# Kernel optimization log

Measured on AMD Instinct MI355X. Metric: run time of the kernel, lower is better.

## Reference

```python
import jax, jax.numpy as jnp
import numpy as np

N_NODES = 100000
N_EDGES = 1600000
IN_DIM, HID_DIM, LAT_DIM = 256, 128, 64


def setup_inputs() -> dict:
    key = jax.random.key(0)
    ks = jax.random.split(key, 10)
    x = jax.random.normal(ks[0], (N_NODES, IN_DIM), dtype=jnp.float32)
    edge_index = jax.random.randint(ks[1], (2, N_EDGES), 0, N_NODES, dtype=jnp.int32)
    s = 1.0 / np.sqrt(IN_DIM)
    W1 = jax.random.normal(ks[2], (IN_DIM, HID_DIM), dtype=jnp.float32) * s
    b1 = jnp.zeros((HID_DIM,), dtype=jnp.float32)
    s2 = 1.0 / np.sqrt(HID_DIM)
    Wmu = jax.random.normal(ks[3], (HID_DIM, LAT_DIM), dtype=jnp.float32) * s2
    bmu = jnp.zeros((LAT_DIM,), dtype=jnp.float32)
    Wls = jax.random.normal(ks[4], (HID_DIM, LAT_DIM), dtype=jnp.float32) * s2
    bls = jnp.zeros((LAT_DIM,), dtype=jnp.float32)
    eps = jax.random.normal(ks[5], (N_NODES, LAT_DIM), dtype=jnp.float32)
    return {"x": x, "edge_index": edge_index, "W1": W1, "b1": b1,
            "Wmu": Wmu, "bmu": bmu, "Wls": Wls, "bls": bls, "eps": eps}


def _gcn_norm(edge_index, n_nodes):
    # PyG GCNConv: add self-loops, symmetric normalization D^-1/2 A D^-1/2
    loops = jnp.arange(n_nodes, dtype=edge_index.dtype)
    src = jnp.concatenate([edge_index[0], loops])
    dst = jnp.concatenate([edge_index[1], loops])
    ones = jnp.ones(src.shape[0], dtype=jnp.float32)
    deg = jax.ops.segment_sum(ones, dst, num_segments=n_nodes)
    dinv = jnp.where(deg > 0, jax.lax.rsqrt(deg), 0.0)
    norm = dinv[src] * dinv[dst]  # [E + N]
    return src, dst, norm


def _gcn_conv(x, src, dst, norm, W, b, n_nodes):
    h = x @ W                       # transform first (in_dim >= out_dim)
    msg = h[src] * norm[:, None]    # gather + scale per edge
    out = jax.ops.segment_sum(msg, dst, num_segments=n_nodes)  # scatter-add
    return out + b


def reference(x, edge_index, W1, b1, Wmu, bmu, Wls, bls, eps):
    n = x.shape[0]
    src, dst, norm = _gcn_norm(edge_index, n)
    hidden = jax.nn.relu(_gcn_conv(x, src, dst, norm, W1, b1, n))
    mu = _gcn_conv(hidden, src, dst, norm, Wmu, bmu, n)
    logstd = _gcn_conv(hidden, src, dst, norm, Wls, bls, n)
    # reparameterize (training mode): z = mu + eps * exp(logstd)
    z = mu + eps * jnp.exp(logstd)
    return (z, mu, logstd)
```

## Files before the change

### kernel.cpp

```cpp
#include <hip/hip_runtime.h>
#include <cstdint>
#include <cstddef>

typedef __attribute__((ext_vector_type(8))) short short8v;
typedef __attribute__((ext_vector_type(4))) float f32x4;

#define BSHIFT 9
#define NBUCK_MAX 256
#define BCAP 16384
#define F8SCALE 16.0f
#define F8INV   0.0625f

__device__ __forceinline__ unsigned short f2bf_rne(float x) {
    unsigned int u = __float_as_uint(x);
    return (unsigned short)((u + 0x7fffu + ((u >> 16) & 1u)) >> 16);
}
__device__ __forceinline__ float bflo(unsigned int u) { return __uint_as_float(u << 16); }
__device__ __forceinline__ float bfhi(unsigned int u) { return __uint_as_float(u & 0xffff0000u); }

__device__ __forceinline__ short8v pack_bf16x8(float4 a, float4 b) {
    unsigned int u0, u1, u2, u3;
    asm("v_cvt_pk_bf16_f32 %0, %1, %2" : "=v"(u0) : "v"(a.x), "v"(a.y));
    asm("v_cvt_pk_bf16_f32 %0, %1, %2" : "=v"(u1) : "v"(a.z), "v"(a.w));
    asm("v_cvt_pk_bf16_f32 %0, %1, %2" : "=v"(u2) : "v"(b.x), "v"(b.y));
    asm("v_cvt_pk_bf16_f32 %0, %1, %2" : "=v"(u3) : "v"(b.z), "v"(b.w));
    uint4 r = make_uint4(u0, u1, u2, u3);
    return *(short8v*)&r;
}

__device__ __forceinline__ unsigned int pk_fp8(float a, float b, float c, float d) {
    int r = 0;
    r = __builtin_amdgcn_cvt_pk_fp8_f32(a, b, r, false);
    r = __builtin_amdgcn_cvt_pk_fp8_f32(c, d, r, true);
    return (unsigned int)r;
}
__device__ __forceinline__ void accf8(float* a, uint2 v) {
    auto p0 = __builtin_amdgcn_cvt_pk_f32_fp8((int)v.x, false);
    auto p1 = __builtin_amdgcn_cvt_pk_f32_fp8((int)v.x, true);
    auto p2 = __builtin_amdgcn_cvt_pk_f32_fp8((int)v.y, false);
    auto p3 = __builtin_amdgcn_cvt_pk_f32_fp8((int)v.y, true);
    a[0] += p0[0]; a[1] += p0[1];
    a[2] += p1[0]; a[3] += p1[1];
    a[4] += p2[0]; a[5] += p2[1];
    a[6] += p3[0]; a[7] += p3[1];
}


__global__ __launch_bounds__(256) void k_scatb(const int* __restrict__ srcv,
                                               const int* __restrict__ dstv,
                                               int* __restrict__ bcur,
                                               unsigned int* __restrict__ ebuf, int E) {
    __shared__ int hcnt[NBUCK_MAX], hbase[NBUCK_MAX], hcur[NBUCK_MAX];
    int t = threadIdx.x;
    for (int b = t; b < NBUCK_MAX; b += 256) { hcnt[b] = 0; hcur[b] = 0; }
    __syncthreads();
    int base = blockIdx.x * 4096;
    for (int q = 0; q < 16; ++q) {
        int i = base + q * 256 + t;
        if (i < E) atomicAdd(&hcnt[dstv[i] >> BSHIFT], 1);
    }
    __syncthreads();
    for (int b = t; b < NBUCK_MAX; b += 256)
        hbase[b] = hcnt[b] ? atomicAdd(&bcur[b], hcnt[b]) : 0;
    __syncthreads();
    for (int q = 0; q < 16; ++q) {
        int i = base + q * 256 + t;
        if (i < E) {
            int d = dstv[i], b = d >> BSHIFT;
            int off = hbase[b] + atomicAdd(&hcur[b], 1);
            if (off < BCAP)
                ebuf[(size_t)b * BCAP + off] = ((unsigned)srcv[i] << 9) | (unsigned)(d & 511);
        }
    }
}

__global__ __launch_bounds__(512) void k_bsort(const unsigned int* __restrict__ ebuf,
                                               const int* __restrict__ bcur,
                                               int* __restrict__ colv,
                                               int* __restrict__ rowstart,
                                               int* __restrict__ rowend,
                                               float* __restrict__ dinv, int n) {
    __shared__ int cnt[512], sc[512], cur[512];
    int t = threadIdx.x;
    int b = blockIdx.x;
    int node0 = b << BSHIFT;
    int nn = min(512, n - node0);
    int s0 = (int)((size_t)b * BCAP);
    int total = min(bcur[b], BCAP);
    cnt[t] = 0;
    __syncthreads();
    for (int i = t; i < total; i += 512)
        atomicAdd(&cnt[ebuf[s0 + i] & 511u], 1);
    __syncthreads();
    int v = cnt[t];
    sc[t] = v;
    __syncthreads();
    for (int off = 1; off < 512; off <<= 1) {
        int x = 0;
        if (t >= off) x = sc[t - off];
        __syncthreads();
        if (t >= off) sc[t] += x;
        __syncthreads();
    }
    if (t < nn) {
        int rs = s0 + sc[t] - v;
        cur[t] = rs;
        rowstart[node0 + t] = rs;
        rowend[node0 + t] = rs + v;
        dinv[node0 + t] = rsqrtf((float)(v + 1));
    }
    __syncthreads();
    for (int i = t; i < total; i += 512) {
        unsigned int pv = ebuf[s0 + i];
        int pos = atomicAdd(&cur[pv & 511u], 1);
        colv[pos] = (int)(pv >> 9);
    }
}


__global__ __launch_bounds__(256) void k_prepB(const float* __restrict__ W1,
                                               const float* __restrict__ Wmu,
                                               const float* __restrict__ Wls,
                                               unsigned short* __restrict__ B1h,
                                               unsigned short* __restrict__ B2h,
                                               int* __restrict__ bcur) {
    int i = blockIdx.x * 256 + threadIdx.x;
    if (blockIdx.x == 0 && threadIdx.x < NBUCK_MAX) bcur[threadIdx.x] = 0;
    if (i < 256 * 128) {
        int k = i >> 7, c = i & 127;
        int ch = ((c & 15) << 3) | (c >> 4);
        B1h[c * 256 + k] = f2bf_rne(W1[k * 128 + ch]);
    }
    if (i < 128 * 128) {
        int k = i >> 7, c = i & 127;
        int ch = ((c & 15) << 3) | (c >> 4);
        float vv = (ch < 64) ? Wmu[k * 64 + ch] : Wls[k * 64 + (ch - 64)];
        B2h[c * 128 + k] = f2bf_rne(vv);
    }
}


__global__ __launch_bounds__(256) void k_gemm1(const float* __restrict__ A,
                                               const unsigned short* __restrict__ Bth,
                                               const float* __restrict__ dinv,
                                               unsigned char* __restrict__ Cf8, int M) {
    const int K = 256;
    __shared__ unsigned short Bs[128 * 128];
    const int tid = threadIdx.x;
    const int w = tid >> 6, l = tid & 63;
    const int lr = l & 15, lq = l >> 4;
    const int row0 = blockIdx.x * 64 + w * 16;

    int rg = row0 + lr;
    const float* ap = A + (size_t)(rg < M ? rg : 0) * K + lq * 8;

    float4 ar[8][2];
#pragma unroll
    for (int s = 0; s < 8; ++s) {
        ar[s][0] = *(const float4*)(ap + s * 32);
        ar[s][1] = *(const float4*)(ap + s * 32 + 4);
    }

    f32x4 acc[8];
#pragma unroll
    for (int ct = 0; ct < 8; ++ct) acc[ct] = (f32x4){0.f, 0.f, 0.f, 0.f};

#pragma unroll
    for (int h = 0; h < 2; ++h) {
        if (h) __syncthreads();
#pragma unroll
        for (int r = 0; r < 8; ++r) {
            int rw = r * 4 + w;
            int sl = rw >> 3, ct = rw & 7;
            short8v v = *(const short8v*)(Bth + (size_t)(ct * 16 + lr) * K + (h * 4 + sl) * 32 + lq * 8);
            *(short8v*)(&Bs[(rw * 64 + l) * 8]) = v;
        }
        __syncthreads();

#pragma unroll
        for (int sl = 0; sl < 4; ++sl) {
            int sg = h * 4 + sl;
            short8v ah = pack_bf16x8(ar[sg][0], ar[sg][1]);
#pragma unroll
            for (int ct = 0; ct < 8; ++ct) {
                short8v bh = *(const short8v*)(&Bs[((sl * 8 + ct) * 64 + l) * 8]);
                acc[ct] = __builtin_amdgcn_mfma_f32_16x16x32_bf16(ah, bh, acc[ct], 0, 0, 0);
            }
        }
    }

    int rbase = row0 + (lq << 2);
#pragma unroll
    for (int j = 0; j < 4; ++j) {
        int row = rbase + j;
        if (row < M) {
            float dv = dinv[row] * F8SCALE;
            uint2 r;
            r.x = pk_fp8(dv * acc[0][j], dv * acc[1][j], dv * acc[2][j], dv * acc[3][j]);
            r.y = pk_fp8(dv * acc[4][j], dv * acc[5][j], dv * acc[6][j], dv * acc[7][j]);
            *(uint2*)(Cf8 + (size_t)row * 128 + lr * 8) = r;
        }
    }
}


__global__ __launch_bounds__(256) void k_prop1(const unsigned char* __restrict__ hf,
                                               const int* __restrict__ colv,
                                               const int* __restrict__ rowstart,
                                               const int* __restrict__ rowend,
                                               const float* __restrict__ dinv,
                                               const float* __restrict__ bias,
                                               unsigned char* __restrict__ of, int n) {
    int wid = (blockIdx.x * 256 + threadIdx.x) >> 6;
    int nid = wid * 4 + ((threadIdx.x >> 4) & 3);
    if (nid >= n) return;
    int cl = threadIdx.x & 15;
    const unsigned char* hp = hf + cl * 8;
    int s = rowstart[nid], e = rowend[nid];
    float a[8] = {0.f, 0.f, 0.f, 0.f, 0.f, 0.f, 0.f, 0.f};
    int i = s;
    for (; i + 4 <= e; i += 4) {
        int c0 = colv[i], c1 = colv[i + 1], c2 = colv[i + 2], c3 = colv[i + 3];
        uint2 v0 = *(const uint2*)(hp + (size_t)c0 * 128);
        uint2 v1 = *(const uint2*)(hp + (size_t)c1 * 128);
        uint2 v2 = *(const uint2*)(hp + (size_t)c2 * 128);
        uint2 v3 = *(const uint2*)(hp + (size_t)c3 * 128);
        accf8(a, v0); accf8(a, v1); accf8(a, v2); accf8(a, v3);
    }
    for (; i < e; ++i) {
        int c = colv[i];
        uint2 v = *(const uint2*)(hp + (size_t)c * 128);
        accf8(a, v);
    }
    uint2 vo = *(const uint2*)(hp + (size_t)nid * 128);
    accf8(a, vo);
    float dv = dinv[nid];
    float din = dv * F8INV;
    float dos = dv * F8SCALE;
    float4 b0 = *(const float4*)(bias + cl * 8);
    float4 b1v = *(const float4*)(bias + cl * 8 + 4);
    float bb[8] = {b0.x, b0.y, b0.z, b0.w, b1v.x, b1v.y, b1v.z, b1v.w};
    float o[8];
#pragma unroll
    for (int k = 0; k < 8; ++k)
        o[k] = fmaxf(a[k] * din + bb[k], 0.f) * dos;
    uint2 r;
    r.x = pk_fp8(o[0], o[1], o[2], o[3]);
    r.y = pk_fp8(o[4], o[5], o[6], o[7]);
    *(uint2*)(of + (size_t)nid * 128 + cl * 8) = r;
}


__global__ __launch_bounds__(256) void k_prop2(const unsigned char* __restrict__ hf,
                                               const int* __restrict__ colv,
                                               const int* __restrict__ rowstart,
                                               const int* __restrict__ rowend,
                                               const float* __restrict__ dinv,
                                               unsigned short* __restrict__ ob, int n) {
    int wid = (blockIdx.x * 256 + threadIdx.x) >> 6;
    int nid = wid * 4 + ((threadIdx.x >> 4) & 3);
    if (nid >= n) return;
    int cl = threadIdx.x & 15;
    const unsigned char* hp = hf + cl * 8;
    int s = rowstart[nid], e = rowend[nid];
    float a[8] = {0.f, 0.f, 0.f, 0.f, 0.f, 0.f, 0.f, 0.f};
    int i = s;
    for (; i + 4 <= e; i += 4) {
        int c0 = colv[i], c1 = colv[i + 1], c2 = colv[i + 2], c3 = colv[i + 3];
        uint2 v0 = *(const uint2*)(hp + (size_t)c0 * 128);
        uint2 v1 = *(const uint2*)(hp + (size_t)c1 * 128);
        uint2 v2 = *(const uint2*)(hp + (size_t)c2 * 128);
        uint2 v3 = *(const uint2*)(hp + (size_t)c3 * 128);
        accf8(a, v0); accf8(a, v1); accf8(a, v2); accf8(a, v3);
    }
    for (; i < e; ++i) {
        int c = colv[i];
        uint2 v = *(const uint2*)(hp + (size_t)c * 128);
        accf8(a, v);
    }
    uint2 vo = *(const uint2*)(hp + (size_t)nid * 128);
    accf8(a, vo);
    float dv = dinv[nid] * F8INV;
    short8v r;
#pragma unroll
    for (int k = 0; k < 8; ++k) r[k] = (short)f2bf_rne(a[k] * dv);
    *(short8v*)(ob + (size_t)nid * 128 + cl * 8) = r;
}


__global__ __launch_bounds__(256) void k_gemm2z(const unsigned short* __restrict__ Ab,
                                                const unsigned short* __restrict__ Bth,
                                                const float* __restrict__ bmu,
                                                const float* __restrict__ bls,
                                                const float* __restrict__ eps,
                                                float* __restrict__ zout,
                                                float* __restrict__ muout,
                                                float* __restrict__ lsout, int M) {
    const int K = 128;
    __shared__ unsigned short Bs[128 * 128];
    const int tid = threadIdx.x;
    const int w = tid >> 6, l = tid & 63;
    const int lr = l & 15, lq = l >> 4;
    const int row0 = blockIdx.x * 128 + w * 32;

    int r0g = row0 + lr, r1g = row0 + 16 + lr;
    const unsigned short* a0p = Ab + (size_t)(r0g < M ? r0g : 0) * K + lq * 8;
    const unsigned short* a1p = Ab + (size_t)(r1g < M ? r1g : 0) * K + lq * 8;

    short8v a0r[4], a1r[4];
#pragma unroll
    for (int s = 0; s < 4; ++s) {
        a0r[s] = *(const short8v*)(a0p + s * 32);
        a1r[s] = *(const short8v*)(a1p + s * 32);
    }

#pragma unroll
    for (int r = 0; r < 8; ++r) {
        int rw = r * 4 + w;
        int s = rw >> 3, ct = rw & 7;
        short8v v = *(const short8v*)(Bth + (size_t)(ct * 16 + lr) * K + s * 32 + lq * 8);
        *(short8v*)(&Bs[(rw * 64 + l) * 8]) = v;
    }
    __syncthreads();

    f32x4 acc[2][8];
#pragma unroll
    for (int rt = 0; rt < 2; ++rt)
#pragma unroll
        for (int ct = 0; ct < 8; ++ct) acc[rt][ct] = (f32x4){0.f, 0.f, 0.f, 0.f};

#pragma unroll
    for (int s = 0; s < 4; ++s) {
#pragma unroll
        for (int ct = 0; ct < 8; ++ct) {
            short8v bh = *(const short8v*)(&Bs[((s * 8 + ct) * 64 + l) * 8]);
            acc[0][ct] = __builtin_amdgcn_mfma_f32_16x16x32_bf16(a0r[s], bh, acc[0][ct], 0, 0, 0);
            acc[1][ct] = __builtin_amdgcn_mfma_f32_16x16x32_bf16(a1r[s], bh, acc[1][ct], 0, 0, 0);
        }
    }

    const bool isMu = (lr < 8);
    float bb[8];
#pragma unroll
    for (int ct = 0; ct < 8; ++ct)
        bb[ct] = isMu ? bmu[lr * 8 + ct] : bls[(lr - 8) * 8 + ct];

#pragma unroll
    for (int rt = 0; rt < 2; ++rt) {
        int rbase = row0 + rt * 16 + (lq << 2);
#pragma unroll
        for (int j = 0; j < 4; ++j) {
            int row = rbase + j;
            float val[8], ex[8], exs[8];
#pragma unroll
            for (int ct = 0; ct < 8; ++ct) {
                val[ct] = acc[rt][ct][j] + bb[ct];
                ex[ct] = __expf(val[ct]);
            }
#pragma unroll
            for (int ct = 0; ct < 8; ++ct) exs[ct] = __shfl(ex[ct], l + 8);
            if (row < M) {
                if (isMu) {
                    size_t o = (size_t)row * 64 + lr * 8;
                    float4 e0 = *(const float4*)(eps + o);
                    float4 e1 = *(const float4*)(eps + o + 4);
                    float epv[8] = {e0.x, e0.y, e0.z, e0.w, e1.x, e1.y, e1.z, e1.w};
                    float z[8];
#pragma unroll
                    for (int ct = 0; ct < 8; ++ct) z[ct] = val[ct] + epv[ct] * exs[ct];
                    *(float4*)(zout + o)     = make_float4(z[0], z[1], z[2], z[3]);
                    *(float4*)(zout + o + 4) = make_float4(z[4], z[5], z[6], z[7]);
                    *(float4*)(muout + o)     = make_float4(val[0], val[1], val[2], val[3]);
                    *(float4*)(muout + o + 4) = make_float4(val[4], val[5], val[6], val[7]);
                } else {
                    size_t o = (size_t)row * 64 + (lr - 8) * 8;
                    *(float4*)(lsout + o)     = make_float4(val[0], val[1], val[2], val[3]);
                    *(float4*)(lsout + o + 4) = make_float4(val[4], val[5], val[6], val[7]);
                }
            }
        }
    }
}


extern "C" void kernel_launch(void* const* d_in, const int* in_sizes, int n_in,
                              void* d_out, int out_size, void* d_ws, size_t ws_size,
                              hipStream_t stream) {
    const float* x   = (const float*)d_in[0];
    const int*   ei  = (const int*)d_in[1];
    const float* W1  = (const float*)d_in[2];
    const float* b1  = (const float*)d_in[3];
    const float* Wmu = (const float*)d_in[4];
    const float* bmu = (const float*)d_in[5];
    const float* Wls = (const float*)d_in[6];
    const float* bls = (const float*)d_in[7];
    const float* eps = (const float*)d_in[8];

    const int n = in_sizes[0] / 256;
    const int E = in_sizes[1] / 2;
    const int* srcv = ei;
    const int* dstv = ei + E;
    const int nbuck = (n + 511) >> BSHIFT;

    char* w = (char*)d_ws;
    auto alloc = [&](size_t bytes) -> char* {
        char* p = w;
        w += (bytes + 255) & ~(size_t)255;
        return p;
    };
    float* dinv     = (float*)alloc((size_t)n * 4);
    int*   rowstart = (int*)alloc((size_t)n * 4);
    int*   rowend   = (int*)alloc((size_t)n * 4);
    int*   bcur     = (int*)alloc((size_t)NBUCK_MAX * 4);
    unsigned int* ebuf = (unsigned int*)alloc((size_t)nbuck * BCAP * 4);
    int*   colv     = (int*)alloc((size_t)nbuck * BCAP * 4);
    unsigned short* B1h = (unsigned short*)alloc(128 * 256 * 2);
    unsigned short* B2h = (unsigned short*)alloc(128 * 128 * 2);
    unsigned char* hf8  = (unsigned char*)alloc((size_t)n * 128);
    unsigned char* hidf8 = (unsigned char*)alloc((size_t)n * 128);
    unsigned short* aggb = (unsigned short*)alloc((size_t)n * 128 * 2);

    const int ecb = (E + 4095) / 4096;

    k_prepB<<<128, 256, 0, stream>>>(W1, Wmu, Wls, B1h, B2h, bcur);
    k_scatb<<<ecb, 256, 0, stream>>>(srcv, dstv, bcur, ebuf, E);
    k_bsort<<<nbuck, 512, 0, stream>>>(ebuf, bcur, colv, rowstart, rowend, dinv, n);

    k_gemm1<<<(n + 63) / 64, 256, 0, stream>>>(x, B1h, dinv, hf8, n);
    k_prop1<<<(n + 15) / 16, 256, 0, stream>>>(hf8, colv, rowstart, rowend, dinv, b1, hidf8, n);
    k_prop2<<<(n + 15) / 16, 256, 0, stream>>>(hidf8, colv, rowstart, rowend, dinv, aggb, n);

    float* zout  = (float*)d_out;
    float* muout = zout + (size_t)n * 64;
    float* lsout = muout + (size_t)n * 64;
    k_gemm2z<<<(n + 127) / 128, 256, 0, stream>>>(aggb, B2h, bmu, bls, eps,
                                                  zout, muout, lsout, n);
}
```

Measured before the change: 194.4 us.

## Fuse second-layer aggregation with mu/logstd GEMM and reparameterization

Merges the prop2 gather-aggregate kernel with the gemm2z kernel. Each 16-node block aggregates into a bf16 tile in shared memory, then runs MFMA against B2t read directly from global memory and writes z, mu and logstd. This removes the global round trip of the 100000x128 bf16 intermediate and one kernel launch. In exchange, each block reloads B2 weights from global or L2, and the output stores become per-lane scalar stores that are less coalesced than the previous float4 layout.

```diff
diff --git a/kernel.cpp b/kernel.cpp
--- a/kernel.cpp
+++ b/kernel.cpp
@@ -15,8 +15,6 @@
     unsigned int u = __float_as_uint(x);
     return (unsigned short)((u + 0x7fffu + ((u >> 16) & 1u)) >> 16);
 }
-__device__ __forceinline__ float bflo(unsigned int u) { return __uint_as_float(u << 16); }
-__device__ __forceinline__ float bfhi(unsigned int u) { return __uint_as_float(u & 0xffff0000u); }
 
 __device__ __forceinline__ short8v pack_bf16x8(float4 a, float4 b) {
     unsigned int u0, u1, u2, u3;
@@ -43,6 +41,27 @@
     a[2] += p1[0]; a[3] += p1[1];
     a[4] += p2[0]; a[5] += p2[1];
     a[6] += p3[0]; a[7] += p3[1];
+}
+
+
+__global__ __launch_bounds__(256) void k_prepB(const float* __restrict__ W1,
+                                               const float* __restrict__ Wmu,
+                                               const float* __restrict__ Wls,
+                                               unsigned short* __restrict__ B1h,
+                                               unsigned short* __restrict__ B2t,
+                                               int* __restrict__ bcur) {
+    int i = blockIdx.x * 256 + threadIdx.x;
+    if (blockIdx.x == 0 && threadIdx.x < NBUCK_MAX) bcur[threadIdx.x] = 0;
+    if (i < 256 * 128) {
+        int k = i >> 7, c = i & 127;
+        int ch = ((c & 15) << 3) | (c >> 4);
+        B1h[c * 256 + k] = f2bf_rne(W1[k * 128 + ch]);
+    }
+    if (i < 128 * 128) {
+        int k = i >> 7, och = i & 127;
+        float vv = (och < 64) ? Wmu[k * 64 + och] : Wls[k * 64 + (och - 64)];
+        B2t[och * 128 + k] = f2bf_rne(vv);
+    }
 }
 
 
@@ -114,28 +133,6 @@
         unsigned int pv = ebuf[s0 + i];
         int pos = atomicAdd(&cur[pv & 511u], 1);
         colv[pos] = (int)(pv >> 9);
-    }
-}
-
-
-__global__ __launch_bounds__(256) void k_prepB(const float* __restrict__ W1,
-                                               const float* __restrict__ Wmu,
-                                               const float* __restrict__ Wls,
-                                               unsigned short* __restrict__ B1h,
-                                               unsigned short* __restrict__ B2h,
-                                               int* __restrict__ bcur) {
-    int i = blockIdx.x * 256 + threadIdx.x;
-    if (blockIdx.x == 0 && threadIdx.x < NBUCK_MAX) bcur[threadIdx.x] = 0;
-    if (i < 256 * 128) {
-        int k = i >> 7, c = i & 127;
-        int ch = ((c & 15) << 3) | (c >> 4);
-        B1h[c * 256 + k] = f2bf_rne(W1[k * 128 + ch]);
-    }
-    if (i < 128 * 128) {
-        int k = i >> 7, c = i & 127;
-        int ch = ((c & 15) << 3) | (c >> 4);
-        float vv = (ch < 64) ? Wmu[k * 64 + ch] : Wls[k * 64 + (ch - 64)];
-        B2h[c * 128 + k] = f2bf_rne(vv);
     }
 }
 
@@ -251,133 +248,82 @@
 }
 
 
-__global__ __launch_bounds__(256) void k_prop2(const unsigned char* __restrict__ hf,
-                                               const int* __restrict__ colv,
-                                               const int* __restrict__ rowstart,
-                                               const int* __restrict__ rowend,
-                                               const float* __restrict__ dinv,
-                                               unsigned short* __restrict__ ob, int n) {
-    int wid = (blockIdx.x * 256 + threadIdx.x) >> 6;
-    int nid = wid * 4 + ((threadIdx.x >> 4) & 3);
-    if (nid >= n) return;
-    int cl = threadIdx.x & 15;
-    const unsigned char* hp = hf + cl * 8;
-    int s = rowstart[nid], e = rowend[nid];
-    float a[8] = {0.f, 0.f, 0.f, 0.f, 0.f, 0.f, 0.f, 0.f};
-    int i = s;
-    for (; i + 4 <= e; i += 4) {
-        int c0 = colv[i], c1 = colv[i + 1], c2 = colv[i + 2], c3 = colv[i + 3];
-        uint2 v0 = *(const uint2*)(hp + (size_t)c0 * 128);
-        uint2 v1 = *(const uint2*)(hp + (size_t)c1 * 128);
-        uint2 v2 = *(const uint2*)(hp + (size_t)c2 * 128);
-        uint2 v3 = *(const uint2*)(hp + (size_t)c3 * 128);
-        accf8(a, v0); accf8(a, v1); accf8(a, v2); accf8(a, v3);
-    }
-    for (; i < e; ++i) {
-        int c = colv[i];
-        uint2 v = *(const uint2*)(hp + (size_t)c * 128);
-        accf8(a, v);
-    }
-    uint2 vo = *(const uint2*)(hp + (size_t)nid * 128);
-    accf8(a, vo);
-    float dv = dinv[nid] * F8INV;
-    short8v r;
-#pragma unroll
-    for (int k = 0; k < 8; ++k) r[k] = (short)f2bf_rne(a[k] * dv);
-    *(short8v*)(ob + (size_t)nid * 128 + cl * 8) = r;
-}
-
-
-__global__ __launch_bounds__(256) void k_gemm2z(const unsigned short* __restrict__ Ab,
-                                                const unsigned short* __restrict__ Bth,
+__global__ __launch_bounds__(256) void k_prop2z(const unsigned char* __restrict__ hf,
+                                                const int* __restrict__ colv,
+                                                const int* __restrict__ rowstart,
+                                                const int* __restrict__ rowend,
+                                                const float* __restrict__ dinv,
+                                                const unsigned short* __restrict__ B2t,
                                                 const float* __restrict__ bmu,
                                                 const float* __restrict__ bls,
                                                 const float* __restrict__ eps,
                                                 float* __restrict__ zout,
                                                 float* __restrict__ muout,
-                                                float* __restrict__ lsout, int M) {
-    const int K = 128;
-    __shared__ unsigned short Bs[128 * 128];
+                                                float* __restrict__ lsout, int n) {
+    __shared__ unsigned short aggb[16][136];
     const int tid = threadIdx.x;
     const int w = tid >> 6, l = tid & 63;
+    const int base = blockIdx.x * 16;
+
+    {
+        int g = l >> 4, cl = l & 15;
+        int slot = w * 4 + g;
+        int nid = base + slot;
+        float a[8] = {0.f, 0.f, 0.f, 0.f, 0.f, 0.f, 0.f, 0.f};
+        float dv = 0.f;
+        if (nid < n) {
+            const unsigned char* hp = hf + cl * 8;
+            int s = rowstart[nid], e = rowend[nid];
+            int i = s;
+            for (; i + 4 <= e; i += 4) {
+                int c0 = colv[i], c1 = colv[i + 1], c2 = colv[i + 2], c3 = colv[i + 3];
+                uint2 v0 = *(const uint2*)(hp + (size_t)c0 * 128);
+                uint2 v1 = *(const uint2*)(hp + (size_t)c1 * 128);
+                uint2 v2 = *(const uint2*)(hp + (size_t)c2 * 128);
+                uint2 v3 = *(const uint2*)(hp + (size_t)c3 * 128);
+                accf8(a, v0); accf8(a, v1); accf8(a, v2); accf8(a, v3);
+            }
+            for (; i < e; ++i) {
+                int c = colv[i];
+                uint2 v = *(const uint2*)(hp + (size_t)c * 128);
+                accf8(a, v);
+            }
+            uint2 vo = *(const uint2*)(hp + (size_t)nid * 128);
+            accf8(a, vo);
+            dv = dinv[nid] * F8INV;
+        }
+        short8v r;
+#pragma unroll
+        for (int k = 0; k < 8; ++k) r[k] = (short)f2bf_rne(a[k] * dv);
+        *(short8v*)(&aggb[slot][cl * 8]) = r;
+    }
+    __syncthreads();
+
     const int lr = l & 15, lq = l >> 4;
-    const int row0 = blockIdx.x * 128 + w * 32;
-
-    int r0g = row0 + lr, r1g = row0 + 16 + lr;
-    const unsigned short* a0p = Ab + (size_t)(r0g < M ? r0g : 0) * K + lq * 8;
-    const unsigned short* a1p = Ab + (size_t)(r1g < M ? r1g : 0) * K + lq * 8;
-
-    short8v a0r[4], a1r[4];
-#pragma unroll
-    for (int s = 0; s < 4; ++s) {
-        a0r[s] = *(const short8v*)(a0p + s * 32);
-        a1r[s] = *(const short8v*)(a1p + s * 32);
-    }
-
-#pragma unroll
-    for (int r = 0; r < 8; ++r) {
-        int rw = r * 4 + w;
-        int s = rw >> 3, ct = rw & 7;
-        short8v v = *(const short8v*)(Bth + (size_t)(ct * 16 + lr) * K + s * 32 + lq * 8);
-        *(short8v*)(&Bs[(rw * 64 + l) * 8]) = v;
-    }
-    __syncthreads();
-
-    f32x4 acc[2][8];
-#pragma unroll
-    for (int rt = 0; rt < 2; ++rt)
-#pragma unroll
-        for (int ct = 0; ct < 8; ++ct) acc[rt][ct] = (f32x4){0.f, 0.f, 0.f, 0.f};
-
-#pragma unroll
-    for (int s = 0; s < 4; ++s) {
-#pragma unroll
-        for (int ct = 0; ct < 8; ++ct) {
-            short8v bh = *(const short8v*)(&Bs[((s * 8 + ct) * 64 + l) * 8]);
-            acc[0][ct] = __builtin_amdgcn_mfma_f32_16x16x32_bf16(a0r[s], bh, acc[0][ct], 0, 0, 0);
-            acc[1][ct] = __builtin_amdgcn_mfma_f32_16x16x32_bf16(a1r[s], bh, acc[1][ct], 0, 0, 0);
-        }
-    }
-
-    const bool isMu = (lr < 8);
-    float bb[8];
-#pragma unroll
-    for (int ct = 0; ct < 8; ++ct)
-        bb[ct] = isMu ? bmu[lr * 8 + ct] : bls[(lr - 8) * 8 + ct];
-
-#pragma unroll
-    for (int rt = 0; rt < 2; ++rt) {
-        int rbase = row0 + rt * 16 + (lq << 2);
-#pragma unroll
-        for (int j = 0; j < 4; ++j) {
-            int row = rbase + j;
-            float val[8], ex[8], exs[8];
-#pragma unroll
-            for (int ct = 0; ct < 8; ++ct) {
-                val[ct] = acc[rt][ct][j] + bb[ct];
-                ex[ct] = __expf(val[ct]);
-            }
-#pragma unroll
-            for (int ct = 0; ct < 8; ++ct) exs[ct] = __shfl(ex[ct], l + 8);
-            if (row < M) {
-                if (isMu) {
-                    size_t o = (size_t)row * 64 + lr * 8;
-                    float4 e0 = *(const float4*)(eps + o);
-                    float4 e1 = *(const float4*)(eps + o + 4);
-                    float epv[8] = {e0.x, e0.y, e0.z, e0.w, e1.x, e1.y, e1.z, e1.w};
-                    float z[8];
-#pragma unroll
-                    for (int ct = 0; ct < 8; ++ct) z[ct] = val[ct] + epv[ct] * exs[ct];
-                    *(float4*)(zout + o)     = make_float4(z[0], z[1], z[2], z[3]);
-                    *(float4*)(zout + o + 4) = make_float4(z[4], z[5], z[6], z[7]);
-                    *(float4*)(muout + o)     = make_float4(val[0], val[1], val[2], val[3]);
-                    *(float4*)(muout + o + 4) = make_float4(val[4], val[5], val[6], val[7]);
-                } else {
-                    size_t o = (size_t)row * 64 + (lr - 8) * 8;
-                    *(float4*)(lsout + o)     = make_float4(val[0], val[1], val[2], val[3]);
-                    *(float4*)(lsout + o + 4) = make_float4(val[4], val[5], val[6], val[7]);
-                }
-            }
+    f32x4 acc0 = (f32x4){0.f, 0.f, 0.f, 0.f};
+    f32x4 acc1 = (f32x4){0.f, 0.f, 0.f, 0.f};
+#pragma unroll
+    for (int sl = 0; sl < 4; ++sl) {
+        short8v af = *(const short8v*)(&aggb[lr][sl * 32 + lq * 8]);
+        short8v b0 = *(const short8v*)(B2t + (size_t)(w * 16 + lr) * 128 + sl * 32 + lq * 8);
+        short8v b1 = *(const short8v*)(B2t + (size_t)((w + 4) * 16 + lr) * 128 + sl * 32 + lq * 8);
+        acc0 = __builtin_amdgcn_mfma_f32_16x16x32_bf16(af, b0, acc0, 0, 0, 0);
+        acc1 = __builtin_amdgcn_mfma_f32_16x16x32_bf16(af, b1, acc1, 0, 0, 0);
+    }
+
+    int och = w * 16 + lr;
+    float bmv = bmu[och], blv = bls[och];
+#pragma unroll
+    for (int j = 0; j < 4; ++j) {
+        int nid = base + lq * 4 + j;
+        if (nid < n) {
+            float mu = acc0[j] + bmv;
+            float ls = acc1[j] + blv;
+            size_t o = (size_t)nid * 64 + och;
+            float z = mu + eps[o] * __expf(ls);
+            zout[o] = z;
+            muout[o] = mu;
+            lsout[o] = ls;
         }
     }
 }
@@ -415,24 +361,23 @@
     unsigned int* ebuf = (unsigned int*)alloc((size_t)nbuck * BCAP * 4);
     int*   colv     = (int*)alloc((size_t)nbuck * BCAP * 4);
     unsigned short* B1h = (unsigned short*)alloc(128 * 256 * 2);
-    unsigned short* B2h = (unsigned short*)alloc(128 * 128 * 2);
-    unsigned char* hf8  = (unsigned char*)alloc((size_t)n * 128);
+    unsigned short* B2t = (unsigned short*)alloc(128 * 128 * 2);
+    unsigned char* hf8   = (unsigned char*)alloc((size_t)n * 128);
     unsigned char* hidf8 = (unsigned char*)alloc((size_t)n * 128);
-    unsigned short* aggb = (unsigned short*)alloc((size_t)n * 128 * 2);
 
     const int ecb = (E + 4095) / 4096;
 
-    k_prepB<<<128, 256, 0, stream>>>(W1, Wmu, Wls, B1h, B2h, bcur);
+    k_prepB<<<128, 256, 0, stream>>>(W1, Wmu, Wls, B1h, B2t, bcur);
     k_scatb<<<ecb, 256, 0, stream>>>(srcv, dstv, bcur, ebuf, E);
     k_bsort<<<nbuck, 512, 0, stream>>>(ebuf, bcur, colv, rowstart, rowend, dinv, n);
 
     k_gemm1<<<(n + 63) / 64, 256, 0, stream>>>(x, B1h, dinv, hf8, n);
     k_prop1<<<(n + 15) / 16, 256, 0, stream>>>(hf8, colv, rowstart, rowend, dinv, b1, hidf8, n);
-    k_prop2<<<(n + 15) / 16, 256, 0, stream>>>(hidf8, colv, rowstart, rowend, dinv, aggb, n);
 
     float* zout  = (float*)d_out;
     float* muout = zout + (size_t)n * 64;
     float* lsout = muout + (size_t)n * 64;
-    k_gemm2z<<<(n + 127) / 128, 256, 0, stream>>>(aggb, B2h, bmu, bls, eps,
-                                                  zout, muout, lsout, n);
-}
+    k_prop2z<<<(n + 15) / 16, 256, 0, stream>>>(hidf8, colv, rowstart, rowend, dinv,
+                                                B2t, bmu, bls, eps,
+                                                zout, muout, lsout, n);
+}
```

Measured after the change: 189.7 us, median of 2. 1.02x faster.
